# Kernel tuning notes

Hardware: AMD Instinct MI355X
Metric: run time of the kernel (lower is better)

## Reference

```python
import jax, jax.numpy as jnp
import numpy as np

B, S, D, H = 2, 2048, 1024, 16
DEPTH = D // H


def setup_inputs() -> dict:
    key = jax.random.key(0)
    ks = jax.random.split(key, 10)
    std = 1.0 / np.sqrt(D)
    v = jax.random.normal(ks[0], (B, S, D), jnp.float32)
    q = jax.random.normal(ks[1], (B, S, D), jnp.float32)
    k = jax.random.normal(ks[2], (B, S, D), jnp.float32)
    # padding mask: 1.0 at masked (padded) key positions, 0.0 elsewhere
    mask = (jax.random.uniform(ks[3], (B, 1, 1, S)) < 0.1).astype(jnp.float32)
    Wq = jax.random.normal(ks[4], (D, D), jnp.float32) * std
    bq = jnp.zeros((D,), jnp.float32)
    Wv = jax.random.normal(ks[5], (D, D), jnp.float32) * std
    bv = jnp.zeros((D,), jnp.float32)
    Wo = jax.random.normal(ks[6], (D, D), jnp.float32) * std
    bo = jnp.zeros((D,), jnp.float32)
    return {"v": v, "q": q, "k": k, "mask": mask,
            "Wq": Wq, "bq": bq, "Wv": Wv, "bv": bv, "Wo": Wo, "bo": bo}


def _split_heads(x):
    # (B, S, D) -> (B, H, S, depth)
    return x.reshape(B, S, H, DEPTH).transpose(0, 2, 1, 3)


def reference(v, q, k, mask, Wq, bq, Wv, bv, Wo, bo):
    # NOTE: faithful to source, keys are projected with the QUERY weights
    # (mixedK = self.wQuery(k) in the original code).
    Q = _split_heads(q @ Wq + bq)
    K = _split_heads(k @ Wq + bq)
    V = _split_heads(v @ Wv + bv)
    scale = 1.0 / jnp.sqrt(jnp.asarray(DEPTH, jnp.float32))
    logits = jnp.einsum('bhqd,bhkd->bhqk', Q, K) * scale
    logits = logits + mask * (-1e9)
    attn = jax.nn.softmax(logits, axis=-1)
    out = jnp.einsum('bhqk,bhkd->bhqd', attn, V)
    out = out.transpose(0, 2, 1, 3).reshape(B, S, D)
    return out @ Wo + bo
```

## Files before the change

kernel.cpp:

```cpp
#include <hip/hip_runtime.h>
#include <cstddef>


namespace {

constexpr int Ss = 2048;
constexpr int Dd = 1024;
constexpr int Mm = 4096;
constexpr float QSCALE = 0.18033688f;
constexpr float NEG2 = -1.442695041e9f;

typedef unsigned short u16;
typedef __attribute__((ext_vector_type(8))) __bf16 bf16x8;
typedef __attribute__((ext_vector_type(4))) float f32x4;
typedef __attribute__((ext_vector_type(16))) float f32x16;
typedef __attribute__((ext_vector_type(4))) unsigned int u32x4;
typedef __attribute__((ext_vector_type(2))) unsigned int u32x2;
typedef __attribute__((ext_vector_type(8))) unsigned short us8;

__device__ __forceinline__ u16 bfc(float f) {
  __bf16 h = (__bf16)f;
  return __builtin_bit_cast(u16, h);
}
__device__ __forceinline__ unsigned pack2(float lo, float hi) {
  return (unsigned)bfc(lo) | ((unsigned)bfc(hi) << 16);
}

__device__ __forceinline__ void gload_lds16(const void* g, void* l) {
  __builtin_amdgcn_global_load_lds(
      (__attribute__((address_space(1))) void*)g,
      (__attribute__((address_space(3))) void*)l, 16, 0, 0);
}

__device__ __forceinline__ f32x4 mfma16(bf16x8 a, bf16x8 b, f32x4 c) {
  return __builtin_amdgcn_mfma_f32_16x16x32_bf16(a, b, c, 0, 0, 0);
}
__device__ __forceinline__ f32x16 mfma32(bf16x8 a, bf16x8 b, f32x16 c) {
  return __builtin_amdgcn_mfma_f32_32x32x16_bf16(a, b, c, 0, 0, 0);
}
__device__ __forceinline__ float exp2_fast(float x) {
  return __builtin_amdgcn_exp2f(x);
}

__device__ __forceinline__ void pl32swap(unsigned& a, unsigned& b) {
#if __has_builtin(__builtin_amdgcn_permlane32_swap)
  u32x2 r = __builtin_amdgcn_permlane32_swap(a, b, false, false);
  a = r[0];
  b = r[1];
#else
  unsigned ax = (unsigned)__shfl_xor((int)a, 32);
  unsigned bx = (unsigned)__shfl_xor((int)b, 32);
  bool hi = (threadIdx.x & 63) >= 32;
  unsigned na = hi ? bx : a;
  unsigned nb = hi ? b : ax;
  a = na;
  b = nb;
#endif
}

#define PIPE_BARRIER_V(N)                                  \
  do {                                                     \
    asm volatile("s_waitcnt vmcnt(" #N ")" ::: "memory");  \
    __builtin_amdgcn_sched_barrier(0);                     \
    __builtin_amdgcn_s_barrier();                          \
    __builtin_amdgcn_sched_barrier(0);                     \
  } while (0)

__device__ __forceinline__ int swz(int row, int col) {
  return row * 64 + ((((col >> 3) ^ (row & 7)) << 3) | (col & 7));
}
__device__ __forceinline__ int src_col(int lane) {
  return ((lane & 7) ^ (lane >> 3)) * 8;
}

__global__ __launch_bounds__(256) void prep(const float* __restrict__ W0,
                                            const float* __restrict__ W1,
                                            const float* __restrict__ W2,
                                            const float* __restrict__ q,
                                            const float* __restrict__ k,
                                            const float* __restrict__ v,
                                            u16* __restrict__ wsbase,
                                            u16* __restrict__ qb,
                                            u16* __restrict__ kb,
                                            u16* __restrict__ vb) {
  __shared__ float tile[32][33];
  const int blk = (int)blockIdx.x;
  const int tid = threadIdx.x;
  if (blk < 3072) {
    const int z = blk >> 10;
    const int rem = blk & 1023;
    const int n0 = (rem & 31) * 32;
    const int k0 = (rem >> 5) * 32;
    const float* W = (z == 0) ? W0 : (z == 1) ? W1 : W2;
    u16* WT = wsbase + (size_t)z * (1024 * 1024);
    const int tx = tid & 31;
    const int ty = tid >> 5;
#pragma unroll
    for (int i = 0; i < 4; ++i)
      tile[ty + i * 8][tx] = W[(size_t)(k0 + ty + i * 8) * 1024 + n0 + tx];
    __syncthreads();
    const int r = tid >> 3;
    const int c4 = (tid & 7) * 4;
    ushort4 o4 = make_ushort4(bfc(tile[c4 + 0][r]), bfc(tile[c4 + 1][r]),
                              bfc(tile[c4 + 2][r]), bfc(tile[c4 + 3][r]));
    *(ushort4*)(&WT[(size_t)(n0 + r) * 1024 + k0 + c4]) = o4;
  } else {
    const int e = blk - 3072;
    const int which = e >> 11;
    const int b2 = e & 2047;
    const float* src = (which == 0) ? q : (which == 1) ? k : v;
    u16* dst = (which == 0) ? qb : (which == 1) ? kb : vb;
    const int base = (b2 * 256 + tid) * 8;
    const float4 a = *(const float4*)(src + base);
    const float4 b = *(const float4*)(src + base + 4);
    us8 o;
    o[0] = bfc(a.x); o[1] = bfc(a.y); o[2] = bfc(a.z); o[3] = bfc(a.w);
    o[4] = bfc(b.x); o[5] = bfc(b.y); o[6] = bfc(b.z); o[7] = bfc(b.w);
    *(us8*)(dst + base) = o;
  }
}

__global__ __launch_bounds__(256) void proj_qkv(
    const u16* __restrict__ qb, const u16* __restrict__ kb,
    const u16* __restrict__ vb, const u16* __restrict__ WqT,
    const u16* __restrict__ WvT, const float* __restrict__ bq,
    const float* __restrict__ bv, const float* __restrict__ maskf,
    u16* __restrict__ Qp, u16* __restrict__ Kp, u16* __restrict__ VpT) {
  constexpr int K = 1024, N = 1024, M = 4096;
  __shared__ u16 As[128 * 64];
  __shared__ u16 Bs[64 * 64];
  const int lin = (int)blockIdx.x;
  const int xcd = lin & 7;
  const int j = lin >> 3;
  const int panel = xcd * 12 + (j >> 4);
  const int ntile = j & 15;
  const int z = panel >> 5;
  const int mtile = panel & 31;
  const int n0 = ntile * 64;
  const int m0 = mtile * 128;

  const u16* A = (z == 0) ? qb : (z == 1) ? kb : vb;
  const u16* Bt = (z == 2) ? WvT : WqT;
  const float* bias = (z == 2) ? bv : bq;
  const float cscale = (z == 0) ? QSCALE : 1.0f;

  const int tid = threadIdx.x;
  const int wid = tid >> 6;
  const int lane = tid & 63;
  const int g = lane >> 4;
  const int lr = lane & 15;

  const f32x4 zero = {0.f, 0.f, 0.f, 0.f};
  f32x4 acc[2][4];
#pragma unroll
  for (int m = 0; m < 2; ++m)
#pragma unroll
    for (int n = 0; n < 4; ++n) acc[m][n] = zero;

  for (int kt = 0; kt < 16; ++kt) {
#pragma unroll
    for (int jj = 0; jj < 4; ++jj) {
      int rb = (wid * 4 + jj) * 8;
      gload_lds16(&A[(size_t)(m0 + rb + (lane >> 3)) * K + kt * 64 + src_col(lane)],
                  &As[rb * 64]);
    }
#pragma unroll
    for (int jj = 0; jj < 2; ++jj) {
      int rb = (wid * 2 + jj) * 8;
      gload_lds16(&Bt[(size_t)(n0 + rb + (lane >> 3)) * K + kt * 64 + src_col(lane)],
                  &Bs[rb * 64]);
    }
    __syncthreads();
#pragma unroll
    for (int kk = 0; kk < 2; ++kk) {
      bf16x8 a[2], b[4];
#pragma unroll
      for (int m = 0; m < 2; ++m)
        a[m] = *(const bf16x8*)(&As[swz(wid * 32 + m * 16 + lr, kk * 32 + g * 8)]);
#pragma unroll
      for (int n = 0; n < 4; ++n)
        b[n] = *(const bf16x8*)(&Bs[swz(n * 16 + lr, kk * 32 + g * 8)]);
#pragma unroll
      for (int m = 0; m < 2; ++m)
#pragma unroll
        for (int n = 0; n < 4; ++n) acc[m][n] = mfma16(a[m], b[n], acc[m][n]);
    }
    __syncthreads();
  }

#pragma unroll
  for (int n = 0; n < 4; ++n) {
    const int col = n0 + n * 16 + lr;
    const float bv_ = bias[col];
#pragma unroll
    for (int m = 0; m < 2; ++m) {
      const int rowb = m0 + wid * 32 + m * 16 + g * 4;
      if (z == 2) {
        const f32x4 mk = *(const f32x4*)(&maskf[rowb]);
        ushort4 o4;
        o4.x = (mk[0] != 0.f) ? (u16)0 : bfc(acc[m][n][0] + bv_);
        o4.y = (mk[1] != 0.f) ? (u16)0 : bfc(acc[m][n][1] + bv_);
        o4.z = (mk[2] != 0.f) ? (u16)0 : bfc(acc[m][n][2] + bv_);
        o4.w = (mk[3] != 0.f) ? (u16)0 : bfc(acc[m][n][3] + bv_);
        *(ushort4*)(&VpT[(size_t)col * M + rowb]) = o4;
      } else {
        u16* Cp = (z == 0) ? Qp : Kp;
#pragma unroll
        for (int r = 0; r < 4; ++r)
          Cp[(size_t)(rowb + r) * N + col] = bfc((acc[m][n][r] + bv_) * cscale);
      }
    }
  }
}

__global__ __launch_bounds__(256) void gemm_o(const u16* __restrict__ Ap,
                                              const u16* __restrict__ Bt,
                                              const float* __restrict__ bias,
                                              float* __restrict__ Cp) {
  constexpr int K = 1024, N = 1024;
  __shared__ u16 As[3][128 * 64];
  __shared__ u16 Bs[3][64 * 64];
  const int lin = (int)blockIdx.x;
  const int xcd = lin & 7;
  const int j = lin >> 3;
  const int mtile = xcd * 4 + (j >> 4);
  const int ntile = j & 15;
  const int n0 = ntile * 64;
  const int m0 = mtile * 128;

  const int tid = threadIdx.x;
  const int wid = tid >> 6;
  const int lane = tid & 63;
  const int g = lane >> 4;
  const int lr = lane & 15;

  const f32x4 zero = {0.f, 0.f, 0.f, 0.f};
  f32x4 acc[2][4];
#pragma unroll
  for (int m = 0; m < 2; ++m)
#pragma unroll
    for (int n = 0; n < 4; ++n) acc[m][n] = zero;

  auto stage = [&](int kt, u16* as, u16* bs) {
#pragma unroll
    for (int jj = 0; jj < 4; ++jj) {
      int rb = (wid * 4 + jj) * 8;
      gload_lds16(&Ap[(size_t)(m0 + rb + (lane >> 3)) * K + kt * 64 + src_col(lane)],
                  as + rb * 64);
    }
#pragma unroll
    for (int jj = 0; jj < 2; ++jj) {
      int rb = (wid * 2 + jj) * 8;
      gload_lds16(&Bt[(size_t)(n0 + rb + (lane >> 3)) * K + kt * 64 + src_col(lane)],
                  bs + rb * 64);
    }
  };

  stage(0, As[0], Bs[0]);
  stage(1, As[1], Bs[1]);

  int b0 = 0;
  for (int kt = 0; kt < 16; ++kt) {
    if (kt < 15) PIPE_BARRIER_V(6);
    else         PIPE_BARRIER_V(0);
    if (kt + 2 < 16) {
      int b2 = b0 + 2; if (b2 >= 3) b2 -= 3;
      stage(kt + 2, As[b2], Bs[b2]);
    }
    const u16* as = As[b0];
    const u16* bs = Bs[b0];
#pragma unroll
    for (int kk = 0; kk < 2; ++kk) {
      bf16x8 a[2], b[4];
#pragma unroll
      for (int m = 0; m < 2; ++m)
        a[m] = *(const bf16x8*)(&as[swz(wid * 32 + m * 16 + lr, kk * 32 + g * 8)]);
#pragma unroll
      for (int n = 0; n < 4; ++n)
        b[n] = *(const bf16x8*)(&bs[swz(n * 16 + lr, kk * 32 + g * 8)]);
#pragma unroll
      for (int m = 0; m < 2; ++m)
#pragma unroll
        for (int n = 0; n < 4; ++n) acc[m][n] = mfma16(a[m], b[n], acc[m][n]);
    }
    b0 = (b0 == 2) ? 0 : b0 + 1;
  }
#pragma unroll
  for (int n = 0; n < 4; ++n) {
    const int col = n0 + n * 16 + lr;
    const float bv_ = bias[col];
#pragma unroll
    for (int m = 0; m < 2; ++m) {
      const int rowb = m0 + wid * 32 + m * 16 + g * 4;
#pragma unroll
      for (int r = 0; r < 4; ++r)
        Cp[(size_t)(rowb + r) * N + col] = acc[m][n][r] + bv_;
    }
  }
}

__global__ __launch_bounds__(512) void attn32(const u16* __restrict__ Qp,
                                              const u16* __restrict__ Kp,
                                              const u16* __restrict__ VpT,
                                              const float* __restrict__ mask,
                                              u16* __restrict__ Op) {
  __shared__ u16 smem[8 * 64 * 64];
  __shared__ float msall[Ss];
  const int tid = threadIdx.x;
  const int wid = tid >> 6;
  const int lane = tid & 63;
  const int l31 = lane & 31;
  const int hi = lane >> 5;
  const int qq = wid & 3;
  const int kh = wid >> 2;
  const int lin = (int)(blockIdx.x + (blockIdx.y << 4));
  const int wl = (lin & 7) * 64 + (lin >> 3);
  const int qt = wl & 15;
  const int bh = wl >> 4;
  const int b = bh >> 4;
  const int h = bh & 15;
  const int q0 = qt * 128;
  const size_t base = ((size_t)b * Ss) * Dd + (size_t)h * 64;
  const size_t vbase = (size_t)h * 64 * Mm + (size_t)b * Ss;
  const int qrow = q0 + qq * 32 + l31;

  auto stageKV = [&](int t, int buf) {
    const int key0 = t * 64;
    const int rb = wid * 8;
    gload_lds16(&Kp[base + (size_t)(key0 + rb + (lane >> 3)) * Dd + src_col(lane)],
                smem + buf * 4096 + rb * 64);
    gload_lds16(&VpT[vbase + (size_t)(rb + (lane >> 3)) * Mm + key0 + src_col(lane)],
                smem + (4 + buf) * 4096 + rb * 64);
  };

  const float4 mk = *(const float4*)(&mask[(size_t)b * Ss + tid * 4]);
  bf16x8 qf[4];
#pragma unroll
  for (int d = 0; d < 4; ++d)
    qf[d] = *(const bf16x8*)(&Qp[base + (size_t)qrow * Dd + d * 16 + hi * 8]);

  stageKV(0, 0);
  stageKV(1, 1);

  {
    f32x4 s = {mk.x * NEG2, mk.y * NEG2, mk.z * NEG2, mk.w * NEG2};
    *(f32x4*)(&msall[tid * 4]) = s;
  }
  asm volatile("s_waitcnt lgkmcnt(0)" ::: "memory");
  __builtin_amdgcn_sched_barrier(0);
  __builtin_amdgcn_s_barrier();
  __builtin_amdgcn_sched_barrier(0);

  f32x16 oacc[2];
#pragma unroll
  for (int i = 0; i < 2; ++i)
#pragma unroll
    for (int r = 0; r < 16; ++r) oacc[i][r] = 0.f;
  float lsum = 0.f;

  for (int i = 0; i < 16; ++i) {
    PIPE_BARRIER_V(0);
    if (i < 15) {
      stageKV(2 * i + 2, (2 * i + 2) & 3);
      stageKV(2 * i + 3, (2 * i + 3) & 3);
    }
#pragma unroll
    for (int u = 0; u < 2; ++u) {
      const int t = 2 * i + u;
      const int buf = t & 3;
      const u16* ks = smem + buf * 4096;
      const u16* vt = smem + (4 + buf) * 4096;
      const float* msp = &msall[t * 64 + kh * 32];

      f32x16 sacc;
#pragma unroll
      for (int a = 0; a < 4; ++a) {
        const f32x4 mv = *(const f32x4*)(&msp[a * 8 + hi * 4]);
#pragma unroll
        for (int jj = 0; jj < 4; ++jj) sacc[a * 4 + jj] = mv[jj];
      }
      __builtin_amdgcn_s_setprio(1);
#pragma unroll
      for (int d = 0; d < 4; ++d) {
        bf16x8 kf = *(const bf16x8*)(&ks[swz(kh * 32 + l31, d * 16 + hi * 8)]);
        sacc = mfma32(kf, qf[d], sacc);
      }
      __builtin_amdgcn_s_setprio(0);

#pragma unroll
      for (int r = 0; r < 16; ++r) sacc[r] = exp2_fast(sacc[r]);

      {
        float sm[8];
#pragma unroll
        for (int r = 0; r < 8; ++r) sm[r] = sacc[r] + sacc[r + 8];
#pragma unroll
        for (int s = 4; s >= 1; s >>= 1)
#pragma unroll
          for (int r = 0; r < s; ++r) sm[r] += sm[r + s];
        lsum += sm[0] + __shfl_xor(sm[0], 32);
      }

      bf16x8 pa[2];
#pragma unroll
      for (int slot = 0; slot < 2; ++slot) {
        const int bse = slot * 8;
        unsigned A0 = pack2(sacc[bse + 0], sacc[bse + 1]);
        unsigned A1 = pack2(sacc[bse + 2], sacc[bse + 3]);
        unsigned B0 = pack2(sacc[bse + 4], sacc[bse + 5]);
        unsigned B1 = pack2(sacc[bse + 6], sacc[bse + 7]);
        pl32swap(A0, B0);
        pl32swap(A1, B1);
        u32x4 w = {A0, A1, B0, B1};
        pa[slot] = __builtin_bit_cast(bf16x8, w);
      }

      __builtin_amdgcn_s_setprio(1);
#pragma unroll
      for (int slot = 0; slot < 2; ++slot)
#pragma unroll
        for (int dsub = 0; dsub < 2; ++dsub) {
          bf16x8 vf = *(const bf16x8*)(
              &vt[swz(dsub * 32 + l31, kh * 32 + slot * 16 + hi * 8)]);
          oacc[dsub] = mfma32(pa[slot], vf, oacc[dsub]);
        }
      __builtin_amdgcn_s_setprio(0);
    }
  }

  __syncthreads();
  float* rbuf = (float*)smem;
  if (kh == 1) {
    float* p = rbuf + qq * 3072 + lane;
#pragma unroll
    for (int r = 0; r < 16; ++r) p[r * 64] = oacc[0][r];
#pragma unroll
    for (int r = 0; r < 16; ++r) p[(16 + r) * 64] = oacc[1][r];
    if (hi == 0) rbuf[12288 + qq * 32 + l31] = lsum;
  }
  __syncthreads();
  if (kh == 0) {
    const float* p = rbuf + qq * 3072 + lane;
#pragma unroll
    for (int r = 0; r < 16; ++r) oacc[0][r] += p[r * 64];
#pragma unroll
    for (int r = 0; r < 16; ++r) oacc[1][r] += p[(16 + r) * 64];
    const float ltot = lsum + rbuf[12288 + qq * 32 + l31];
    float* lrow = rbuf + 12800 + qq * 32;
    if (hi == 0) lrow[l31] = __builtin_amdgcn_rcpf(ltot);
    f32x4 rl[4];
#pragma unroll
    for (int a = 0; a < 4; ++a)
      rl[a] = *(const f32x4*)(&lrow[a * 8 + hi * 4]);
#pragma unroll
    for (int dsub = 0; dsub < 2; ++dsub) {
      const int col = h * 64 + dsub * 32 + l31;
#pragma unroll
      for (int r = 0; r < 16; ++r) {
        const int row = q0 + qq * 32 + (r & 3) + 8 * (r >> 2) + 4 * hi;
        Op[((size_t)b * Ss + row) * Dd + col] =
            bfc(oacc[dsub][r] * rl[r >> 2][r & 3]);
      }
    }
  }
}

}

extern "C" void kernel_launch(void* const* d_in, const int* in_sizes, int n_in,
                              void* d_out, int out_size, void* d_ws, size_t ws_size,
                              hipStream_t stream) {
  (void)in_sizes; (void)n_in; (void)out_size; (void)ws_size;
  const float* v = (const float*)d_in[0];
  const float* q = (const float*)d_in[1];
  const float* k = (const float*)d_in[2];
  const float* mask = (const float*)d_in[3];
  const float* Wq = (const float*)d_in[4];
  const float* bq = (const float*)d_in[5];
  const float* Wv = (const float*)d_in[6];
  const float* bv = (const float*)d_in[7];
  const float* Wo = (const float*)d_in[8];
  const float* bo = (const float*)d_in[9];
  float* out = (float*)d_out;

  constexpr size_t MEG = 1024 * 1024;
  u16* ws = (u16*)d_ws;
  u16* WqT = ws;
  u16* WvT = ws + 1 * MEG;
  u16* WoT = ws + 2 * MEG;
  u16* qb  = ws + 3 * MEG;
  u16* kb  = ws + 7 * MEG;
  u16* vb  = ws + 11 * MEG;
  u16* Qp  = ws + 15 * MEG;
  u16* Kp  = ws + 19 * MEG;
  u16* VpT = ws + 23 * MEG;
  u16* AO  = qb;

  prep<<<dim3(3072 + 6144), 256, 0, stream>>>(Wq, Wv, Wo, q, k, v, ws, qb, kb, vb);
  proj_qkv<<<dim3(1536), 256, 0, stream>>>(qb, kb, vb, WqT, WvT, bq, bv, mask,
                                           Qp, Kp, VpT);
  attn32<<<dim3(16, 32), 512, 0, stream>>>(Qp, Kp, VpT, mask, AO);
  gemm_o<<<dim3(512), 256, 0, stream>>>(AO, WoT, bo, out);
}
```

Before: 119.3 us.

## Shrink output GEMM tile to 64x64 with 32x32 MFMA and no multi-buffering

The output projection GEMM moves from 128x64 tiles with a triple-buffered async pipeline and 16x16 MFMAs to 64x64 tiles using 32x32x16 MFMAs. Each wave now owns one 32x32 accumulator, and a single LDS buffer is used with barriers before and after compute. Grid size doubles to 1024 blocks to raise occupancy and parallelism, and LDS use per block drops. The cost is that load latency is no longer hidden by prefetching and each tile reuses less data.

```diff
diff --git a/kernel.cpp b/kernel.cpp
--- a/kernel.cpp
+++ b/kernel.cpp
@@ -218,84 +218,51 @@
                                               const float* __restrict__ bias,
                                               float* __restrict__ Cp) {
   constexpr int K = 1024, N = 1024;
-  __shared__ u16 As[3][128 * 64];
-  __shared__ u16 Bs[3][64 * 64];
+  __shared__ u16 As[64 * 64];
+  __shared__ u16 Bs[64 * 64];
   const int lin = (int)blockIdx.x;
   const int xcd = lin & 7;
   const int j = lin >> 3;
-  const int mtile = xcd * 4 + (j >> 4);
+  const int mtile = xcd * 8 + (j >> 4);
   const int ntile = j & 15;
   const int n0 = ntile * 64;
-  const int m0 = mtile * 128;
+  const int m0 = mtile * 64;
 
   const int tid = threadIdx.x;
   const int wid = tid >> 6;
   const int lane = tid & 63;
-  const int g = lane >> 4;
-  const int lr = lane & 15;
-
-  const f32x4 zero = {0.f, 0.f, 0.f, 0.f};
-  f32x4 acc[2][4];
-#pragma unroll
-  for (int m = 0; m < 2; ++m)
-#pragma unroll
-    for (int n = 0; n < 4; ++n) acc[m][n] = zero;
-
-  auto stage = [&](int kt, u16* as, u16* bs) {
-#pragma unroll
-    for (int jj = 0; jj < 4; ++jj) {
-      int rb = (wid * 4 + jj) * 8;
+  const int l31 = lane & 31;
+  const int hi = lane >> 5;
+  const int wr = wid >> 1, wc = wid & 1;
+
+  f32x16 acc;
+#pragma unroll
+  for (int r = 0; r < 16; ++r) acc[r] = 0.f;
+
+  for (int kt = 0; kt < 16; ++kt) {
+#pragma unroll
+    for (int jj = 0; jj < 2; ++jj) {
+      const int rb = (wid * 2 + jj) * 8;
       gload_lds16(&Ap[(size_t)(m0 + rb + (lane >> 3)) * K + kt * 64 + src_col(lane)],
-                  as + rb * 64);
-    }
-#pragma unroll
-    for (int jj = 0; jj < 2; ++jj) {
-      int rb = (wid * 2 + jj) * 8;
+                  &As[rb * 64]);
       gload_lds16(&Bt[(size_t)(n0 + rb + (lane >> 3)) * K + kt * 64 + src_col(lane)],
-                  bs + rb * 64);
-    }
-  };
-
-  stage(0, As[0], Bs[0]);
-  stage(1, As[1], Bs[1]);
-
-  int b0 = 0;
-  for (int kt = 0; kt < 16; ++kt) {
-    if (kt < 15) PIPE_BARRIER_V(6);
-    else         PIPE_BARRIER_V(0);
-    if (kt + 2 < 16) {
-      int b2 = b0 + 2; if (b2 >= 3) b2 -= 3;
-      stage(kt + 2, As[b2], Bs[b2]);
-    }
-    const u16* as = As[b0];
-    const u16* bs = Bs[b0];
-#pragma unroll
-    for (int kk = 0; kk < 2; ++kk) {
-      bf16x8 a[2], b[4];
-#pragma unroll
-      for (int m = 0; m < 2; ++m)
-        a[m] = *(const bf16x8*)(&as[swz(wid * 32 + m * 16 + lr, kk * 32 + g * 8)]);
-#pragma unroll
-      for (int n = 0; n < 4; ++n)
-        b[n] = *(const bf16x8*)(&bs[swz(n * 16 + lr, kk * 32 + g * 8)]);
-#pragma unroll
-      for (int m = 0; m < 2; ++m)
-#pragma unroll
-        for (int n = 0; n < 4; ++n) acc[m][n] = mfma16(a[m], b[n], acc[m][n]);
-    }
-    b0 = (b0 == 2) ? 0 : b0 + 1;
-  }
-#pragma unroll
-  for (int n = 0; n < 4; ++n) {
-    const int col = n0 + n * 16 + lr;
-    const float bv_ = bias[col];
-#pragma unroll
-    for (int m = 0; m < 2; ++m) {
-      const int rowb = m0 + wid * 32 + m * 16 + g * 4;
-#pragma unroll
-      for (int r = 0; r < 4; ++r)
-        Cp[(size_t)(rowb + r) * N + col] = acc[m][n][r] + bv_;
-    }
+                  &Bs[rb * 64]);
+    }
+    __syncthreads();
+#pragma unroll
+    for (int d = 0; d < 4; ++d) {
+      bf16x8 af = *(const bf16x8*)(&As[swz(wr * 32 + l31, d * 16 + hi * 8)]);
+      bf16x8 bf = *(const bf16x8*)(&Bs[swz(wc * 32 + l31, d * 16 + hi * 8)]);
+      acc = mfma32(af, bf, acc);
+    }
+    __syncthreads();
+  }
+  const int col = n0 + wc * 32 + l31;
+  const float bv_ = bias[col];
+#pragma unroll
+  for (int r = 0; r < 16; ++r) {
+    const int row = m0 + wr * 32 + (r & 3) + 8 * (r >> 2) + 4 * hi;
+    Cp[(size_t)row * N + col] = acc[r] + bv_;
   }
 }
 
@@ -500,5 +467,5 @@
   proj_qkv<<<dim3(1536), 256, 0, stream>>>(qb, kb, vb, WqT, WvT, bq, bv, mask,
                                            Qp, Kp, VpT);
   attn32<<<dim3(16, 32), 512, 0, stream>>>(Qp, Kp, VpT, mask, AO);
-  gemm_o<<<dim3(512), 256, 0, stream>>>(AO, WoT, bo, out);
-}
+  gemm_o<<<dim3(1024), 256, 0, stream>>>(AO, WoT, bo, out);
+}
```

Result: no change. 119.8 us (+0.5%).
